# Performance work log

Measured on AMD Instinct MI355X. Metric: run time of the kernel, lower is better.

Reference implementation:

```python
import jax, jax.numpy as jnp
import numpy as np

D = 1024
N_PASSES = 2


def _hadamard(d):
    # Sylvester construction: d must be a power of 2
    H = np.array([[1.0]], dtype=np.float32)
    while H.shape[0] < d:
        H = np.block([[H, H], [H, -H]])
    return H


def setup_inputs() -> dict:
    key = jax.random.key(0)
    kx, ks = jax.random.split(key)
    x = jax.random.normal(kx, (8, 8192, D), dtype=jnp.float32)
    # random +/-1 sign vectors, one per pass
    signs = jnp.where(jax.random.bernoulli(ks, 0.5, (N_PASSES, D)), 1.0, -1.0).astype(jnp.float32)
    h_mat = jnp.asarray(_hadamard(D))  # unnormalized Walsh-Hadamard matrix [D, D]
    return {"x": x, "signs": signs, "h_mat": h_mat}


def reference(x, signs, h_mat):
    # Cascaded SRHT: (sign flip -> WHT -> scale by 1/sqrt(d)) x n_passes
    d = x.shape[-1]
    scale = 1.0 / jnp.sqrt(jnp.asarray(d, dtype=x.dtype))
    out = x
    for i in range(N_PASSES):
        out = (out * signs[i]) @ h_mat * scale
    return out
```

## Files before the change

### kernel.cpp

```cpp
#include <hip/hip_runtime.h>

#define DD 1024

__device__ __forceinline__ void fwht16(float (&v)[16]) {
  #pragma unroll
  for (int h = 1; h < 16; h <<= 1) {
    #pragma unroll
    for (int i = 0; i < 16; ++i) {
      if (!(i & h)) {
        float a = v[i], b = v[i | h];
        v[i]     = a + b;
        v[i | h] = a - b;
      }
    }
  }
}

__device__ __forceinline__ void shfl_stage(float (&v)[16], int mask, int lane) {
  const float sgn = (lane & mask) ? -1.0f : 1.0f;
  #pragma unroll
  for (int j = 0; j < 16; ++j) {
    float o = __shfl_xor(v[j], mask, 64);
    v[j] = fmaf(sgn, v[j], o);
  }
}

__global__ __launch_bounds__(256) void srht_kernel(
    const float* __restrict__ x,
    const float* __restrict__ signs,
    float* __restrict__ out)
{
  __shared__ float lds[4][DD + DD / 32];
  const int lane = threadIdx.x & 63;
  const int wv   = threadIdx.x >> 6;
  const long row = (long)blockIdx.x * 4 + wv;

  const float* __restrict__ xr = x + row * DD;
  float* __restrict__ orow     = out + row * DD;
  const float* __restrict__ s0 = signs;
  const float* __restrict__ s1 = signs + DD;
  float* buf = lds[wv];

  float v[16];

  {
    const float4* xp = (const float4*)(xr + 16 * lane);
    const float4* sp = (const float4*)(s0 + 16 * lane);
    #pragma unroll
    for (int c = 0; c < 4; ++c) {
      float4 a = xp[c], s = sp[c];
      v[4 * c + 0] = a.x * s.x;
      v[4 * c + 1] = a.y * s.y;
      v[4 * c + 2] = a.z * s.z;
      v[4 * c + 3] = a.w * s.w;
    }
  }

  fwht16(v);
  shfl_stage(v, 1, lane);
  shfl_stage(v, 2, lane);

  {
    const int wb = 16 * lane + (lane >> 1);
    #pragma unroll
    for (int j = 0; j < 16; ++j) buf[wb + j] = v[j];
  }
  __syncthreads();
  {
    const int rb = lane + (lane >> 5);
    #pragma unroll
    for (int k = 0; k < 16; ++k) v[k] = buf[rb + 66 * k];
  }
  fwht16(v);

  #pragma unroll
  for (int k = 0; k < 16; ++k)
    v[k] *= s1[lane + 64 * k] * 0.03125f;

  fwht16(v);
  __syncthreads();
  {
    const int wb = lane + (lane >> 5);
    #pragma unroll
    for (int k = 0; k < 16; ++k) buf[wb + 66 * k] = v[k];
  }
  __syncthreads();
  {
    const int rb = 16 * lane + (lane >> 1);
    #pragma unroll
    for (int j = 0; j < 16; ++j) v[j] = buf[rb + j];
  }
  shfl_stage(v, 1, lane);
  shfl_stage(v, 2, lane);
  fwht16(v);

  {
    float4* op = (float4*)(orow + 16 * lane);
    #pragma unroll
    for (int c = 0; c < 4; ++c) {
      float4 r;
      r.x = v[4 * c + 0] * 0.03125f;
      r.y = v[4 * c + 1] * 0.03125f;
      r.z = v[4 * c + 2] * 0.03125f;
      r.w = v[4 * c + 3] * 0.03125f;
      op[c] = r;
    }
  }
}

extern "C" void kernel_launch(void* const* d_in, const int* in_sizes, int n_in,
                              void* d_out, int out_size, void* d_ws, size_t ws_size,
                              hipStream_t stream) {
  const float* x     = (const float*)d_in[0];
  const float* signs = (const float*)d_in[1];
  float* out         = (float*)d_out;

  const int rows   = in_sizes[0] / DD;
  const int blocks = rows / 4;

  hipLaunchKernelGGL(srht_kernel, dim3(blocks), dim3(256), 0, stream,
                     x, signs, out);
}
```

Measured before the change: 122.9 us.

## Swizzle wave-private LDS transpose, drop barriers, use nontemporal global access

Replaces the padded LDS transpose with an XOR-swizzled layout. This allows 128-bit vector LDS writes and reads in the row-major phases while avoiding bank conflicts in the strided phases. Because each wave only touches its own LDS slice, the block-wide __syncthreads barriers are removed. The second-pass sign vector is loaded into registers up front, and x and out now use nontemporal loads and stores to reduce cache pollution in this streaming kernel. The risks are the correctness of the swizzle index math and relying on in-order LDS access within a wave once the barriers are gone.

```diff
diff --git a/kernel.cpp b/kernel.cpp
--- a/kernel.cpp
+++ b/kernel.cpp
@@ -1,6 +1,8 @@
 #include <hip/hip_runtime.h>
 
 #define DD 1024
+
+typedef float f32x4 __attribute__((ext_vector_type(4)));
 
 __device__ __forceinline__ void fwht16(float (&v)[16]) {
   #pragma unroll
@@ -30,7 +32,7 @@
     const float* __restrict__ signs,
     float* __restrict__ out)
 {
-  __shared__ float lds[4][DD + DD / 32];
+  __shared__ float lds[4][DD];
   const int lane = threadIdx.x & 63;
   const int wv   = threadIdx.x >> 6;
   const long row = (long)blockIdx.x * 4 + wv;
@@ -41,14 +43,28 @@
   const float* __restrict__ s1 = signs + DD;
   float* buf = lds[wv];
 
+  const int lu = lane >> 4;
+  const int hb = (lane >> 5) & 1;
+  const int m  = (lane >> 2) & 3;
+  const int t  = lane & 3;
+  const int base_e = 16 * lu + 4 * (m ^ hb) + t;
+  const int base_o = 16 * lu + 4 * (m ^ ((hb + 2) & 3)) + t;
+  const int qL    = (lane >> 1) & 3;
+  const int abase = 16 * lane;
+
+  float s1v[16];
+  #pragma unroll
+  for (int k = 0; k < 16; ++k) s1v[k] = s1[lane + 64 * k];
+
   float v[16];
 
   {
-    const float4* xp = (const float4*)(xr + 16 * lane);
-    const float4* sp = (const float4*)(s0 + 16 * lane);
+    const f32x4* xp = (const f32x4*)(xr + 16 * lane);
+    const f32x4* sp = (const f32x4*)(s0 + 16 * lane);
     #pragma unroll
     for (int c = 0; c < 4; ++c) {
-      float4 a = xp[c], s = sp[c];
+      f32x4 a = __builtin_nontemporal_load(xp + c);
+      f32x4 s = sp[c];
       v[4 * c + 0] = a.x * s.x;
       v[4 * c + 1] = a.y * s.y;
       v[4 * c + 2] = a.z * s.z;
@@ -60,50 +76,48 @@
   shfl_stage(v, 1, lane);
   shfl_stage(v, 2, lane);
 
-  {
-    const int wb = 16 * lane + (lane >> 1);
-    #pragma unroll
-    for (int j = 0; j < 16; ++j) buf[wb + j] = v[j];
+  #pragma unroll
+  for (int c = 0; c < 4; ++c) {
+    f32x4 w4 = {v[4 * c], v[4 * c + 1], v[4 * c + 2], v[4 * c + 3]};
+    *(f32x4*)(buf + abase + 4 * (c ^ qL)) = w4;
   }
-  __syncthreads();
-  {
-    const int rb = lane + (lane >> 5);
-    #pragma unroll
-    for (int k = 0; k < 16; ++k) v[k] = buf[rb + 66 * k];
-  }
+  #pragma unroll
+  for (int k = 0; k < 16; ++k)
+    v[k] = buf[((k & 1) ? base_o : base_e) + 64 * k];
+
+  fwht16(v);
+
+  #pragma unroll
+  for (int k = 0; k < 16; ++k) v[k] *= s1v[k] * 0.03125f;
+
   fwht16(v);
 
   #pragma unroll
   for (int k = 0; k < 16; ++k)
-    v[k] *= s1[lane + 64 * k] * 0.03125f;
+    buf[((k & 1) ? base_o : base_e) + 64 * k] = v[k];
+  #pragma unroll
+  for (int c = 0; c < 4; ++c) {
+    f32x4 r4 = *(const f32x4*)(buf + abase + 4 * (c ^ qL));
+    v[4 * c + 0] = r4.x;
+    v[4 * c + 1] = r4.y;
+    v[4 * c + 2] = r4.z;
+    v[4 * c + 3] = r4.w;
+  }
 
-  fwht16(v);
-  __syncthreads();
-  {
-    const int wb = lane + (lane >> 5);
-    #pragma unroll
-    for (int k = 0; k < 16; ++k) buf[wb + 66 * k] = v[k];
-  }
-  __syncthreads();
-  {
-    const int rb = 16 * lane + (lane >> 1);
-    #pragma unroll
-    for (int j = 0; j < 16; ++j) v[j] = buf[rb + j];
-  }
   shfl_stage(v, 1, lane);
   shfl_stage(v, 2, lane);
   fwht16(v);
 
   {
-    float4* op = (float4*)(orow + 16 * lane);
+    f32x4* op = (f32x4*)(orow + 16 * lane);
     #pragma unroll
     for (int c = 0; c < 4; ++c) {
-      float4 r;
+      f32x4 r;
       r.x = v[4 * c + 0] * 0.03125f;
       r.y = v[4 * c + 1] * 0.03125f;
       r.z = v[4 * c + 2] * 0.03125f;
       r.w = v[4 * c + 3] * 0.03125f;
-      op[c] = r;
+      __builtin_nontemporal_store(r, op + c);
     }
   }
 }
```

New measurement: 377.6 us. 3.07x slower.
